# Performance work log

Hardware: AMD Instinct MI355X
Metric: run time of the kernel (lower is better)

Reference implementation:

```python
import jax, jax.numpy as jnp
import numpy as np

B, T, C, N = 2, 2048, 4096, 4096

def setup_inputs() -> dict:
    key = jax.random.key(0)
    k1, k2, k3, k4 = jax.random.split(key, 4)
    y = jax.random.normal(k1, (B, T, C), dtype=jnp.float32)
    # quantized weight: uint8 codes in [0,255], stored/used as float after upcast
    weight = jnp.round(jax.random.uniform(k2, (C, N), dtype=jnp.float32) * 255.0)
    rng = jax.random.uniform(k3, (1, 1, C), dtype=jnp.float32) * 0.01  # per-input-channel scale
    offset = jax.random.normal(k4, (C,), dtype=jnp.float32) * 0.01    # per-input-channel offset
    return {"y": y, "weight": weight, "rng": rng, "offset": offset}

def reference(y, weight, rng, offset):
    # yv = y.reshape(-1,C) @ offset -> [B,T,1] correction term
    yv = jnp.einsum('btc,c->bt', y, offset)[..., None]
    # (y * range) @ weight  (dequantized GEMM) + correction
    out = jnp.einsum('btc,cn->btn', y * rng, weight) + yv
    return out
```

## Files before the change

kernel.cpp:

```cpp
#include <hip/hip_runtime.h>

typedef unsigned short u16;
typedef unsigned int u32;
typedef unsigned char u8;
typedef signed char i8;

typedef int i32x4 __attribute__((ext_vector_type(4)));

__device__ inline void gld16(const i8* g, i8* l) {
    __builtin_amdgcn_global_load_lds((const __attribute__((address_space(1))) void*)g,
                                     (__attribute__((address_space(3))) void*)l,
                                     16, 0, 0);
}

__global__ __launch_bounds__(256) void prep_kernel(const float* __restrict__ y,
                                                   const float* __restrict__ rng,
                                                   const float* __restrict__ off,
                                                   const float* __restrict__ w,
                                                   uint4* __restrict__ qy,
                                                   uint4* __restrict__ wq,
                                                   float* __restrict__ sp,
                                                   float* __restrict__ tv) {
    __shared__ i8 tile[64][68];
    __shared__ float ra[4], rs1[4], rs2[4];
    const int tid = threadIdx.x;

    if (blockIdx.x < 4096) {
        const int row = blockIdx.x;
        const float* yr = y + (size_t)row * 4096;
        const int base = tid * 16;

        float ysr[16];
        float amax = 0.0f, s1 = 0.0f, s2 = 0.0f;
        #pragma unroll
        for (int ii = 0; ii < 4; ++ii) {
            float4 v = *(const float4*)&yr[base + ii * 4];
            float4 g = *(const float4*)&rng[base + ii * 4];
            float4 o = *(const float4*)&off[base + ii * 4];
            float p0 = v.x * g.x, p1 = v.y * g.y, p2 = v.z * g.z, p3 = v.w * g.w;
            ysr[ii * 4 + 0] = p0; ysr[ii * 4 + 1] = p1;
            ysr[ii * 4 + 2] = p2; ysr[ii * 4 + 3] = p3;
            s1 += p0 + p1 + p2 + p3;
            s2 += v.x * o.x + v.y * o.y + v.z * o.z + v.w * o.w;
            amax = fmaxf(amax, fmaxf(fmaxf(fabsf(p0), fabsf(p1)), fmaxf(fabsf(p2), fabsf(p3))));
        }
        #pragma unroll
        for (int d = 32; d > 0; d >>= 1) {
            amax = fmaxf(amax, __shfl_down(amax, d));
            s1 += __shfl_down(s1, d);
            s2 += __shfl_down(s2, d);
        }
        const int wv = tid >> 6;
        if ((tid & 63) == 0) { ra[wv] = amax; rs1[wv] = s1; rs2[wv] = s2; }
        __syncthreads();
        const float sm = fmaxf(fmaxf(ra[0], ra[1]), fmaxf(ra[2], ra[3]));
        const float inv = sm > 0.0f ? 127.0f / sm : 0.0f;

        u32 d[4];
        #pragma unroll
        for (int g = 0; g < 4; ++g) {
            u32 b0 = (u8)(i8)(int)rintf(ysr[g * 4 + 0] * inv);
            u32 b1 = (u8)(i8)(int)rintf(ysr[g * 4 + 1] * inv);
            u32 b2 = (u8)(i8)(int)rintf(ysr[g * 4 + 2] * inv);
            u32 b3 = (u8)(i8)(int)rintf(ysr[g * 4 + 3] * inv);
            d[g] = b0 | (b1 << 8) | (b2 << 16) | (b3 << 24);
        }
        const int j = (tid & 7) ^ (row & 7);
        qy[(size_t)row * 256 + (tid >> 3) * 8 + j] = make_uint4(d[0], d[1], d[2], d[3]);
        if (tid == 0) {
            sp[row] = sm / 127.0f;
            tv[row] = 128.0f * (rs1[0] + rs1[1] + rs1[2] + rs1[3])
                            + (rs2[0] + rs2[1] + rs2[2] + rs2[3]);
        }
    } else {
        const int bid = blockIdx.x - 4096;
        const int n0 = (bid & 63) * 64;
        const int k0 = (bid >> 6) * 64;
        const int c4 = tid & 15;
        const int r0 = tid >> 4;
        #pragma unroll
        for (int i = 0; i < 4; ++i) {
            int kk = r0 + i * 16;
            float4 v = *(const float4*)&w[(size_t)(k0 + kk) * 4096 + n0 + c4 * 4];
            u32 b0 = (u8)(i8)((int)v.x - 128);
            u32 b1 = (u8)(i8)((int)v.y - 128);
            u32 b2 = (u8)(i8)((int)v.z - 128);
            u32 b3 = (u8)(i8)((int)v.w - 128);
            *(u32*)&tile[kk][c4 * 4] = b0 | (b1 << 8) | (b2 << 16) | (b3 << 24);
        }
        __syncthreads();
        const int nl = tid >> 2;
        const int ci = tid & 3;
        const int l = ((k0 >> 4) & 7) + ci;
        const int j = l ^ ((n0 + nl) & 7);
        u32 d[4];
        #pragma unroll
        for (int g = 0; g < 4; ++g) {
            int kl = ci * 16 + g * 4;
            d[g] = (u32)(u8)tile[kl + 0][nl] | ((u32)(u8)tile[kl + 1][nl] << 8)
                 | ((u32)(u8)tile[kl + 2][nl] << 16) | ((u32)(u8)tile[kl + 3][nl] << 24);
        }
        wq[(size_t)(n0 + nl) * 256 + (k0 >> 7) * 8 + j] = make_uint4(d[0], d[1], d[2], d[3]);
    }
}

__global__ __launch_bounds__(512, 2) void gemm_kernel(const i8* __restrict__ qy,
                                                      const i8* __restrict__ wq,
                                                      const float* __restrict__ sp,
                                                      const float* __restrict__ tv,
                                                      float* __restrict__ out) {
    __shared__ i8 As[2][256 * 128];
    __shared__ i8 Bs[2][256 * 128];

    const int bid = blockIdx.x;
    const int xcd = bid & 7;
    const int jj = bid >> 3;
    const int bn = (xcd * 2 + (jj & 1)) * 256;
    const int bm = (jj >> 1) * 256;

    const int tid = (int)threadIdx.x;
    const int lane = tid & 63;
    const int wv = tid >> 6;
    const int wm = (wv >> 2) * 128;
    const int wn = (wv & 3) * 64;
    const int r = lane & 15;
    const int q = lane >> 4;
    const int col0 = (q ^ (r & 7)) << 4;

    const int offA0 = (wm + r) * 128 + col0;
    const int offB0 = (wn + r) * 128 + col0;
    const int offA1 = offA0 ^ 64;
    const int offB1 = offB0 ^ 64;

    const int rsub = lane >> 3;
    const int jsub = lane & 7;
    const i8* gA[4]; const i8* gB[4];
    int ldso[4];
    #pragma unroll
    for (int c = 0; c < 4; ++c) {
        const int ca = wv * 4 + c;
        gA[c] = qy + (size_t)(bm + ca * 8 + rsub) * 4096 + jsub * 16;
        gB[c] = wq + (size_t)(bn + ca * 8 + rsub) * 4096 + jsub * 16;
        ldso[c] = ca * 1024;
    }

    i32x4 acc[8][4] = {};
    i32x4 a[4][2], b[4][2];

    #pragma unroll
    for (int c = 0; c < 4; ++c) { gld16(gA[c], &As[0][ldso[c]]); gA[c] += 128; }
    #pragma unroll
    for (int c = 0; c < 4; ++c) { gld16(gB[c], &Bs[0][ldso[c]]); gB[c] += 128; }
    asm volatile("s_waitcnt vmcnt(0)" ::: "memory");
    __builtin_amdgcn_s_barrier();

#define RD_A4(RB, MB)                                                         \
    _Pragma("unroll")                                                         \
    for (int mi = 0; mi < 4; ++mi) {                                          \
        a[mi][0] = *(const i32x4*)&As[RB][offA0 + (MB + mi) * 2048];          \
        a[mi][1] = *(const i32x4*)&As[RB][offA1 + (MB + mi) * 2048];          \
    }
#define RD_B2(RB, NB)                                                         \
    _Pragma("unroll")                                                         \
    for (int ni = 0; ni < 2; ++ni) {                                          \
        b[NB + ni][0] = *(const i32x4*)&Bs[RB][offB0 + (NB + ni) * 2048];     \
        b[NB + ni][1] = *(const i32x4*)&Bs[RB][offB1 + (NB + ni) * 2048];     \
    }
#define MM16(MB, NB)                                                          \
    _Pragma("unroll")                                                         \
    for (int mi = 0; mi < 4; ++mi) {                                          \
        _Pragma("unroll")                                                     \
        for (int ni = 0; ni < 2; ++ni) {                                      \
            acc[MB + mi][NB + ni] = __builtin_amdgcn_mfma_i32_16x16x64_i8(    \
                a[mi][0], b[NB + ni][0], acc[MB + mi][NB + ni], 0, 0, 0);     \
            acc[MB + mi][NB + ni] = __builtin_amdgcn_mfma_i32_16x16x64_i8(    \
                a[mi][1], b[NB + ni][1], acc[MB + mi][NB + ni], 0, 0, 0);     \
        }                                                                     \
    }
#define WAIT_LGKM do { asm volatile("s_waitcnt lgkmcnt(0)" ::: "memory");     \
                       __builtin_amdgcn_sched_barrier(0); } while (0)

#define KTILE(RB, WB, PF)                                                     \
    do {                                                                      \
                                                  \
        RD_A4(RB, 0); RD_B2(RB, 0);                                           \
        if (PF) {                                                             \
            _Pragma("unroll")                                                 \
            for (int c = 0; c < 4; ++c) { gld16(gA[c], &As[WB][ldso[c]]); gA[c] += 128; } \
        }                                                                     \
        __builtin_amdgcn_s_barrier(); WAIT_LGKM;                              \
        __builtin_amdgcn_s_setprio(1); MM16(0, 0); __builtin_amdgcn_s_setprio(0); \
        __builtin_amdgcn_s_barrier();                                         \
                                                            \
        RD_B2(RB, 2);                                                         \
        if (PF) {                                                             \
            _Pragma("unroll")                                                 \
            for (int c = 0; c < 4; ++c) { gld16(gB[c], &Bs[WB][ldso[c]]); gB[c] += 128; } \
        }                                                                     \
        __builtin_amdgcn_s_barrier(); WAIT_LGKM;                              \
        __builtin_amdgcn_s_setprio(1); MM16(0, 2); __builtin_amdgcn_s_setprio(0); \
        __builtin_amdgcn_s_barrier();                                         \
                                  \
        RD_A4(RB, 4);                                                         \
        __builtin_amdgcn_s_barrier(); WAIT_LGKM;                              \
        __builtin_amdgcn_s_setprio(1); MM16(4, 0); __builtin_amdgcn_s_setprio(0); \
        __builtin_amdgcn_s_barrier();                                         \
                  \
        __builtin_amdgcn_s_setprio(1); MM16(4, 2); __builtin_amdgcn_s_setprio(0); \
        asm volatile("s_waitcnt vmcnt(0)" ::: "memory");                      \
        __builtin_amdgcn_s_barrier();                                         \
    } while (0)

    #pragma unroll 1
    for (int t = 0; t < 15; ++t) {
        KTILE(0, 1, 1);
        KTILE(1, 0, 1);
    }
    KTILE(0, 1, 1);
    KTILE(1, 0, 0);

#undef KTILE
#undef WAIT_LGKM
#undef MM16
#undef RD_B2
#undef RD_A4

    #pragma unroll
    for (int mi = 0; mi < 8; ++mi) {
        #pragma unroll
        for (int rr = 0; rr < 4; ++rr) {
            const int gm = bm + wm + mi * 16 + q * 4 + rr;
            const float sc = sp[gm];
            const float tt = tv[gm];
            #pragma unroll
            for (int ni = 0; ni < 4; ++ni) {
                const int gn = bn + wn + ni * 16 + r;
                out[(size_t)gm * 4096 + gn] = sc * (float)acc[mi][ni][rr] + tt;
            }
        }
    }
}

extern "C" void kernel_launch(void* const* d_in, const int* in_sizes, int n_in,
                              void* d_out, int out_size, void* d_ws, size_t ws_size,
                              hipStream_t stream) {
    const float* y   = (const float*)d_in[0];
    const float* w   = (const float*)d_in[1];
    const float* rng = (const float*)d_in[2];
    const float* off = (const float*)d_in[3];
    float* out = (float*)d_out;

    i8* qy = (i8*)d_ws;
    i8* wq = qy + (size_t)4096 * 4096;
    float* sp = (float*)(wq + (size_t)4096 * 4096);
    float* tv = sp + 4096;

    prep_kernel<<<8192, 256, 0, stream>>>(y, rng, off, w, (uint4*)qy, (uint4*)wq, sp, tv);
    gemm_kernel<<<256, 512, 0, stream>>>(qy, wq, sp, tv, out);
}
```

Before: 239.9 us.

## Restructure int8 GEMM K-tile pipeline into two phases with partial vmcnt waits

Collapses the four-phase K-tile schedule into two phases, each loading all four B fragments and doing a 4x4 MFMA block. Global-to-LDS prefetches are split into halves staged across the phases, with partial vmcnt waits replacing the full drain at the end of each tile. The global load mapping is reorganized so that A and B staging follows the half-tile split. The goal is fewer barriers and more overlap of global loads with MFMA work, at the cost of more live B registers and more fragile wait-count correctness.

```diff
diff --git a/kernel.cpp b/kernel.cpp
--- a/kernel.cpp
+++ b/kernel.cpp
@@ -134,24 +134,30 @@
 
     const int rsub = lane >> 3;
     const int jsub = lane & 7;
-    const i8* gA[4]; const i8* gB[4];
-    int ldso[4];
-    #pragma unroll
-    for (int c = 0; c < 4; ++c) {
-        const int ca = wv * 4 + c;
-        gA[c] = qy + (size_t)(bm + ca * 8 + rsub) * 4096 + jsub * 16;
-        gB[c] = wq + (size_t)(bn + ca * 8 + rsub) * 4096 + jsub * 16;
-        ldso[c] = ca * 1024;
-    }
+    const i8* aP0 = qy + (size_t)(bm + wv * 8 + rsub) * 4096 + jsub * 16;
+    const i8* bP0 = wq + (size_t)(bn + (wv >> 2) * 64 + (wv & 3) * 8 + rsub) * 4096 + jsub * 16;
+    const int lAo = wv * 1024 + lane * 16;
+    const int lBo = (wv >> 2) * 8192 + (wv & 3) * 1024 + lane * 16;
+
+    size_t koff = 0;
+
+#define STAGE_A(WB, H) do {                                                   \
+        gld16(aP0 + koff + (size_t)((H) * 64) * 4096,       &As[WB][lAo + (H) * 8192]);          \
+        gld16(aP0 + koff + (size_t)((H) * 64 + 128) * 4096, &As[WB][lAo + (H) * 8192 + 16384]);  \
+    } while (0)
+#define STAGE_B(WB, H) do {                                                   \
+        gld16(bP0 + koff + (size_t)((H) * 32) * 4096,       &Bs[WB][lBo + (H) * 4096]);          \
+        gld16(bP0 + koff + (size_t)((H) * 32 + 128) * 4096, &Bs[WB][lBo + (H) * 4096 + 16384]);  \
+    } while (0)
 
     i32x4 acc[8][4] = {};
     i32x4 a[4][2], b[4][2];
 
-    #pragma unroll
-    for (int c = 0; c < 4; ++c) { gld16(gA[c], &As[0][ldso[c]]); gA[c] += 128; }
-    #pragma unroll
-    for (int c = 0; c < 4; ++c) { gld16(gB[c], &Bs[0][ldso[c]]); gB[c] += 128; }
-    asm volatile("s_waitcnt vmcnt(0)" ::: "memory");
+    STAGE_A(0, 0); STAGE_B(0, 0); STAGE_B(0, 1);
+    __builtin_amdgcn_sched_barrier(0);
+    STAGE_A(0, 1);
+    koff = 128;
+    asm volatile("s_waitcnt vmcnt(2)" ::: "memory");
     __builtin_amdgcn_s_barrier();
 
 #define RD_A4(RB, MB)                                                         \
@@ -160,55 +166,46 @@
         a[mi][0] = *(const i32x4*)&As[RB][offA0 + (MB + mi) * 2048];          \
         a[mi][1] = *(const i32x4*)&As[RB][offA1 + (MB + mi) * 2048];          \
     }
-#define RD_B2(RB, NB)                                                         \
+#define RD_B4(RB)                                                             \
     _Pragma("unroll")                                                         \
-    for (int ni = 0; ni < 2; ++ni) {                                          \
-        b[NB + ni][0] = *(const i32x4*)&Bs[RB][offB0 + (NB + ni) * 2048];     \
-        b[NB + ni][1] = *(const i32x4*)&Bs[RB][offB1 + (NB + ni) * 2048];     \
-    }
-#define MM16(MB, NB)                                                          \
+    for (int ni = 0; ni < 4; ++ni) {                                          \
+        b[ni][0] = *(const i32x4*)&Bs[RB][offB0 + ni * 2048];                 \
+        b[ni][1] = *(const i32x4*)&Bs[RB][offB1 + ni * 2048];                 \
+    }
+#define MM32(MB)                                                              \
     _Pragma("unroll")                                                         \
     for (int mi = 0; mi < 4; ++mi) {                                          \
         _Pragma("unroll")                                                     \
-        for (int ni = 0; ni < 2; ++ni) {                                      \
-            acc[MB + mi][NB + ni] = __builtin_amdgcn_mfma_i32_16x16x64_i8(    \
-                a[mi][0], b[NB + ni][0], acc[MB + mi][NB + ni], 0, 0, 0);     \
-            acc[MB + mi][NB + ni] = __builtin_amdgcn_mfma_i32_16x16x64_i8(    \
-                a[mi][1], b[NB + ni][1], acc[MB + mi][NB + ni], 0, 0, 0);     \
+        for (int ni = 0; ni < 4; ++ni) {                                      \
+            acc[MB + mi][ni] = __builtin_amdgcn_mfma_i32_16x16x64_i8(         \
+                a[mi][0], b[ni][0], acc[MB + mi][ni], 0, 0, 0);               \
+            acc[MB + mi][ni] = __builtin_amdgcn_mfma_i32_16x16x64_i8(         \
+                a[mi][1], b[ni][1], acc[MB + mi][ni], 0, 0, 0);               \
         }                                                                     \
     }
-#define WAIT_LGKM do { asm volatile("s_waitcnt lgkmcnt(0)" ::: "memory");     \
-                       __builtin_amdgcn_sched_barrier(0); } while (0)
 
 #define KTILE(RB, WB, PF)                                                     \
     do {                                                                      \
-                                                  \
-        RD_A4(RB, 0); RD_B2(RB, 0);                                           \
-        if (PF) {                                                             \
-            _Pragma("unroll")                                                 \
-            for (int c = 0; c < 4; ++c) { gld16(gA[c], &As[WB][ldso[c]]); gA[c] += 128; } \
-        }                                                                     \
-        __builtin_amdgcn_s_barrier(); WAIT_LGKM;                              \
-        __builtin_amdgcn_s_setprio(1); MM16(0, 0); __builtin_amdgcn_s_setprio(0); \
+                          \
+        RD_A4(RB, 0);                                                         \
+        RD_B4(RB);                                                            \
+        if (PF) { STAGE_A(WB, 0); STAGE_B(WB, 0); }                           \
+        asm volatile("s_waitcnt lgkmcnt(0)" ::: "memory");                    \
+        __builtin_amdgcn_sched_barrier(0);                                    \
+        __builtin_amdgcn_s_setprio(1); MM32(0); __builtin_amdgcn_s_setprio(0); \
+        if (PF) asm volatile("s_waitcnt vmcnt(4)" ::: "memory");   \
+        else    asm volatile("s_waitcnt vmcnt(0)" ::: "memory");              \
         __builtin_amdgcn_s_barrier();                                         \
-                                                            \
-        RD_B2(RB, 2);                                                         \
-        if (PF) {                                                             \
-            _Pragma("unroll")                                                 \
-            for (int c = 0; c < 4; ++c) { gld16(gB[c], &Bs[WB][ldso[c]]); gB[c] += 128; } \
-        }                                                                     \
-        __builtin_amdgcn_s_barrier(); WAIT_LGKM;                              \
-        __builtin_amdgcn_s_setprio(1); MM16(0, 2); __builtin_amdgcn_s_setprio(0); \
+                    \
+        RD_A4(RB, 4);                                                         \
+        if (PF) { STAGE_B(WB, 1); __builtin_amdgcn_sched_barrier(0); STAGE_A(WB, 1); } \
+        asm volatile("s_waitcnt lgkmcnt(0)" ::: "memory");                    \
+        __builtin_amdgcn_sched_barrier(0);                                    \
+        __builtin_amdgcn_s_setprio(1); MM32(4); __builtin_amdgcn_s_setprio(0); \
+        if (PF) asm volatile("s_waitcnt vmcnt(2)" ::: "memory");   \
+        else    asm volatile("s_waitcnt vmcnt(0)" ::: "memory");              \
         __builtin_amdgcn_s_barrier();                                         \
-                                  \
-        RD_A4(RB, 4);                                                         \
-        __builtin_amdgcn_s_barrier(); WAIT_LGKM;                              \
-        __builtin_amdgcn_s_setprio(1); MM16(4, 0); __builtin_amdgcn_s_setprio(0); \
-        __builtin_amdgcn_s_barrier();                                         \
-                  \
-        __builtin_amdgcn_s_setprio(1); MM16(4, 2); __builtin_amdgcn_s_setprio(0); \
-        asm volatile("s_waitcnt vmcnt(0)" ::: "memory");                      \
-        __builtin_amdgcn_s_barrier();                                         \
+        koff += 128;                                                          \
     } while (0)
 
     #pragma unroll 1
@@ -220,10 +217,11 @@
     KTILE(1, 0, 0);
 
 #undef KTILE
-#undef WAIT_LGKM
-#undef MM16
-#undef RD_B2
+#undef MM32
+#undef RD_B4
 #undef RD_A4
+#undef STAGE_B
+#undef STAGE_A
 
     #pragma unroll
     for (int mi = 0; mi < 8; ++mi) {
```

Result: no change. 238.5 us (-0.6%).
